# Optimization experiments

Hardware: AMD Instinct MI355X
Metric: run time of the kernel (lower is better)

Reference implementation:

```python
import jax, jax.numpy as jnp
import numpy as np

N_HEAD = 12
D_HEAD = 64


def setup_inputs() -> dict:
    key = jax.random.key(0)
    ks = jax.random.split(key, 9)
    bs, seq, d_model = 4, 2048, 768
    sc = 1.0 / np.sqrt(d_model)
    return {
        "q": jax.random.normal(ks[0], (bs, seq, d_model), jnp.float32),
        "k": jax.random.normal(ks[1], (bs, seq, d_model), jnp.float32),
        "v": jax.random.normal(ks[2], (bs, seq, d_model), jnp.float32),
        "Wq": jax.random.normal(ks[3], (d_model, d_model), jnp.float32) * sc,
        "bq": jax.random.normal(ks[4], (d_model,), jnp.float32) * 0.01,
        "Wk": jax.random.normal(ks[5], (d_model, d_model), jnp.float32) * sc,
        "bk": jax.random.normal(ks[6], (d_model,), jnp.float32) * 0.01,
        "Wv": jax.random.normal(ks[7], (d_model, d_model), jnp.float32) * sc,
        "bv": jax.random.normal(ks[8], (d_model,), jnp.float32) * 0.01,
    }


def _split_heads(x):
    # [bs, seq, n_head*d_head] -> [bs, n_head, seq, d_head]
    bs, seq, _ = x.shape
    return x.reshape(bs, seq, N_HEAD, D_HEAD).transpose(0, 2, 1, 3)


def reference(q, k, v, Wq, bq, Wk, bk, Wv, bv):
    # Linear projections (torch Linear: x @ W.T + b)
    wq = _split_heads(q @ Wq.T + bq)
    wk = _split_heads(k @ Wk.T + bk)
    wv = _split_heads(v @ Wv.T + bv)
    # scale=False in defaults -> raw dot products, no mask, dropout is eval no-op
    scores = jnp.einsum("bhqd,bhkd->bhqk", wq, wk)  # [bs, h, S, S]
    probs = jax.nn.softmax(scores, axis=-1)
    attn_vec = jnp.einsum("bhqk,bhkd->bhqd", probs, wv)
    bs, _, seq, _ = attn_vec.shape
    # merge heads -> [bs, seq, n_head*d_head]
    return attn_vec.transpose(0, 2, 1, 3).reshape(bs, seq, N_HEAD * D_HEAD)
```

## Files before the change

kernel.cpp:

```cpp
#include <hip/hip_runtime.h>
#include <stdint.h>

typedef _Float16 half8  __attribute__((ext_vector_type(8)));
typedef _Float16 half4v __attribute__((ext_vector_type(4)));
typedef float    floatx4 __attribute__((ext_vector_type(4)));

#define LOG2E 1.44269504088896340736f

__device__ __forceinline__ void gl_lds16(const _Float16* g, _Float16* l) {
  __builtin_amdgcn_global_load_lds(
      (__attribute__((address_space(1))) void*)g,
      (__attribute__((address_space(3))) void*)l, 16, 0, 0);
}

__device__ __forceinline__ half4v pack4(float a, float b, float c, float d) {
  auto lo = __builtin_amdgcn_cvt_pkrtz(a, b);
  auto hi = __builtin_amdgcn_cvt_pkrtz(c, d);
  return half4v{static_cast<_Float16>(lo[0]), static_cast<_Float16>(lo[1]),
                static_cast<_Float16>(hi[0]), static_cast<_Float16>(hi[1])};
}

struct CvtArgs {
  const float* sx[3];
  const float* sw[3];
  _Float16*    dx;
  _Float16*    dw;
};

__global__ void cvt_kernel(CvtArgs a) {
  const int z  = blockIdx.y;
  const int bx = blockIdx.x;
  const float* src;
  _Float16*    dst;
  int base;
  if (bx < 3072) { src = a.sx[z]; dst = a.dx + (size_t)z * 6291456; base = bx * 2048; }
  else           { src = a.sw[z]; dst = a.dw + (size_t)z * 589824;  base = (bx - 3072) * 2048; }
  const int i = base + threadIdx.x * 8;
  const float4* s = (const float4*)(src + i);
  float4 v0 = s[0], v1 = s[1];
  half8 h = { (_Float16)v0.x, (_Float16)v0.y, (_Float16)v0.z, (_Float16)v0.w,
              (_Float16)v1.x, (_Float16)v1.y, (_Float16)v1.z, (_Float16)v1.w };
  *(half8*)(dst + i) = h;
}


__device__ __forceinline__ void gemm_stage16(const _Float16* __restrict__ P,
                                             _Float16* sb, int r0, int k0, int tid) {
  #pragma unroll
  for (int i = 0; i < 2; ++i) {
    int G = i * 256 + tid;
    int r = G >> 2, gl = G & 3;
    int g = gl ^ ((r >> 1) & 3);
    gl_lds16(P + (size_t)(r0 + r) * 768 + k0 + g * 8, sb + G * 8);
  }
}

template <int RB, int WB, int VM, bool PREF>
__device__ __forceinline__ void gemm_body(
    int kpre, const _Float16* __restrict__ X, const _Float16* __restrict__ W,
    _Float16* As, _Float16* Bs, int m0, int n0, int tid, int z,
    int wr, int wc, int qd, int col, floatx4 (&acc)[4][4])
{
  asm volatile("s_waitcnt vmcnt(%0)" :: "i"(VM) : "memory");
  __builtin_amdgcn_s_barrier();
  __builtin_amdgcn_sched_barrier(0);
  if (PREF) {
    gemm_stage16(X, As + WB * 4096, m0, kpre, tid);
    gemm_stage16(W, Bs + WB * 4096, n0, kpre, tid);
  }
  __builtin_amdgcn_sched_barrier(0);

  half8 af[4], bf[4];
  #pragma unroll
  for (int t = 0; t < 4; ++t) {
    int ra = wr * 64 + t * 16 + col;
    af[t] = *(const half8*)(As + RB * 4096 + ra * 32 + ((qd ^ ((ra >> 1) & 3)) * 8));
  }
  #pragma unroll
  for (int t = 0; t < 4; ++t) {
    int rb = wc * 64 + t * 16 + col;
    bf[t] = *(const half8*)(Bs + RB * 4096 + rb * 32 + ((qd ^ ((rb >> 1) & 3)) * 8));
  }
  if (z == 2) {
    #pragma unroll
    for (int i = 0; i < 4; ++i)
      #pragma unroll
      for (int j = 0; j < 4; ++j)
        acc[i][j] = __builtin_amdgcn_mfma_f32_16x16x32_f16(af[i], bf[j], acc[i][j], 0, 0, 0);
  } else {
    #pragma unroll
    for (int i = 0; i < 4; ++i)
      #pragma unroll
      for (int j = 0; j < 4; ++j)
        acc[i][j] = __builtin_amdgcn_mfma_f32_16x16x32_f16(bf[j], af[i], acc[i][j], 0, 0, 0);
  }
}

__global__ __launch_bounds__(256, 2) void qkv_gemm(
    const _Float16* __restrict__ xh,
    const _Float16* __restrict__ wh,
    const float* __restrict__ bqp, const float* __restrict__ bkp, const float* __restrict__ bvp,
    _Float16* __restrict__ oq, _Float16* __restrict__ ok, _Float16* __restrict__ ovt)
{
  __shared__ __attribute__((aligned(16))) char smem[49152];
  _Float16* As = (_Float16*)smem;
  _Float16* Bs = (_Float16*)(smem + 24576);
  _Float16* Es = (_Float16*)smem;

  const int flat = blockIdx.x;
  const int z    = flat / 384;
  const int f    = flat % 384;
  const int xcd  = f & 7;
  const int slot = f >> 3;
  const int n0 = (slot % 6) * 128;
  const int m0 = (xcd + 8 * (slot / 6)) * 128;

  const _Float16* X = xh + (size_t)z * 6291456;
  const _Float16* W = wh + (size_t)z * 589824;
  const int tid  = threadIdx.x;
  const int lane = tid & 63, wid = tid >> 6;
  const int wr = wid >> 1, wc = wid & 1;
  const int qd = lane >> 4, col = lane & 15;

  const floatx4 z4 = {0.f, 0.f, 0.f, 0.f};
  floatx4 acc[4][4];
  #pragma unroll
  for (int i = 0; i < 4; ++i)
    #pragma unroll
    for (int j = 0; j < 4; ++j) acc[i][j] = z4;

  gemm_stage16(X, As,        m0, 0,  tid);
  gemm_stage16(W, Bs,        n0, 0,  tid);
  gemm_stage16(X, As + 4096, m0, 32, tid);
  gemm_stage16(W, Bs + 4096, n0, 32, tid);

  int jn = 64;
  #pragma unroll 1
  for (int it = 0; it < 7; ++it) {
    gemm_body<0, 2, 4, true>(jn,      X, W, As, Bs, m0, n0, tid, z, wr, wc, qd, col, acc);
    gemm_body<1, 0, 4, true>(jn + 32, X, W, As, Bs, m0, n0, tid, z, wr, wc, qd, col, acc);
    gemm_body<2, 1, 4, true>(jn + 64, X, W, As, Bs, m0, n0, tid, z, wr, wc, qd, col, acc);
    jn += 96;
  }
  gemm_body<0, 2, 4, true >(736, X, W, As, Bs, m0, n0, tid, z, wr, wc, qd, col, acc);
  gemm_body<1, 0, 4, false>(0,   X, W, As, Bs, m0, n0, tid, z, wr, wc, qd, col, acc);
  gemm_body<2, 1, 0, false>(0,   X, W, As, Bs, m0, n0, tid, z, wr, wc, qd, col, acc);

  __syncthreads();

  const float* bias = (z == 0) ? bqp : ((z == 1) ? bkp : bvp);
  const int b = m0 >> 11, s0 = m0 & 2047;
  if (z == 2) {
    #pragma unroll
    for (int j = 0; j < 4; ++j) {
      int n_loc = wc * 64 + j * 16 + col;
      float bb = bias[n0 + n_loc];
      #pragma unroll
      for (int i = 0; i < 4; ++i) {
        int s_loc = wr * 64 + i * 16 + qd * 4;
        half4v h = pack4(acc[i][j][0] + bb, acc[i][j][1] + bb,
                         acc[i][j][2] + bb, acc[i][j][3] + bb);
        *(half4v*)(Es + n_loc * 160 + s_loc) = h;
      }
    }
    __syncthreads();
    #pragma unroll
    for (int it = 0; it < 8; ++it) {
      int row = it * 16 + (tid >> 4);
      int k   = tid & 15;
      half8 vr = *(const half8*)(Es + row * 160 + k * 8);
      *(half8*)(ovt + ((size_t)(b * 768 + n0 + row)) * 2048 + s0 + k * 8) = vr;
    }
  } else {
    _Float16* O = (z == 0) ? oq : ok;
    const float scale = (z == 0) ? LOG2E : 1.0f;
    #pragma unroll
    for (int j = 0; j < 4; ++j) {
      int n_loc = wc * 64 + j * 16 + qd * 4;
      float4 bb = *(const float4*)(bias + n0 + n_loc);
      #pragma unroll
      for (int i = 0; i < 4; ++i) {
        int s_loc = wr * 64 + i * 16 + col;
        half4v h = pack4((acc[i][j][0] + bb.x) * scale, (acc[i][j][1] + bb.y) * scale,
                         (acc[i][j][2] + bb.z) * scale, (acc[i][j][3] + bb.w) * scale);
        *(half4v*)(Es + s_loc * 160 + n_loc) = h;
      }
    }
    __syncthreads();
    const int hh0 = n0 >> 6;
    #pragma unroll
    for (int it = 0; it < 8; ++it) {
      int seg = it * 32 + (tid >> 3);
      int s = seg >> 1, hseg = seg & 1;
      int k = tid & 7;
      half8 vr = *(const half8*)(Es + s * 160 + hseg * 64 + k * 8);
      int mb = (m0 + s) >> 11, sg = (m0 + s) & 2047;
      *(half8*)(O + (size_t)(mb * 12 + hh0 + hseg) * 131072
                  + (size_t)sg * 64 + k * 8) = vr;
    }
  }
}


__device__ __forceinline__ void issue_panel(const float* __restrict__ P,
                                            int r0, int k0, int tid,
                                            float4& a0, float4& a1,
                                            float4& b0, float4& b1) {
  {
    int G = tid;
    int r = G >> 2, gl = G & 3;
    int g = gl ^ ((r >> 1) & 3);
    const float4* s = (const float4*)(P + (size_t)(r0 + r) * 768 + k0 + g * 8);
    a0 = s[0]; a1 = s[1];
  }
  {
    int G = 256 + tid;
    int r = G >> 2, gl = G & 3;
    int g = gl ^ ((r >> 1) & 3);
    const float4* s = (const float4*)(P + (size_t)(r0 + r) * 768 + k0 + g * 8);
    b0 = s[0]; b1 = s[1];
  }
}

__device__ __forceinline__ void write_panel(_Float16* sb, int tid,
                                            const float4& a0, const float4& a1,
                                            const float4& b0, const float4& b1) {
  half8 h0 = { (_Float16)a0.x, (_Float16)a0.y, (_Float16)a0.z, (_Float16)a0.w,
               (_Float16)a1.x, (_Float16)a1.y, (_Float16)a1.z, (_Float16)a1.w };
  *(half8*)(sb + tid * 8) = h0;
  half8 h1 = { (_Float16)b0.x, (_Float16)b0.y, (_Float16)b0.z, (_Float16)b0.w,
               (_Float16)b1.x, (_Float16)b1.y, (_Float16)b1.z, (_Float16)b1.w };
  *(half8*)(sb + (256 + tid) * 8) = h1;
}

template <int BUF>
__device__ __forceinline__ void gemm_body_f32(
    int knext, const float* __restrict__ X, const float* __restrict__ W,
    _Float16* As, _Float16* Bs, int m0, int n0, int tid, int z,
    int wr, int wc, int qd, int col, floatx4 (&acc)[4][4])
{
  const bool pref = (knext < 768);
  float4 xa0, xa1, xb0, xb1, wa0, wa1, wb0, wb1;
  if (pref) {
    issue_panel(X, m0, knext, tid, xa0, xa1, xb0, xb1);
    issue_panel(W, n0, knext, tid, wa0, wa1, wb0, wb1);
  }

  half8 af[4], bf[4];
  #pragma unroll
  for (int t = 0; t < 4; ++t) {
    int ra = wr * 64 + t * 16 + col;
    af[t] = *(const half8*)(As + BUF * 4096 + ra * 32 + ((qd ^ ((ra >> 1) & 3)) * 8));
  }
  #pragma unroll
  for (int t = 0; t < 4; ++t) {
    int rb = wc * 64 + t * 16 + col;
    bf[t] = *(const half8*)(Bs + BUF * 4096 + rb * 32 + ((qd ^ ((rb >> 1) & 3)) * 8));
  }
  if (z == 2) {
    #pragma unroll
    for (int i = 0; i < 4; ++i)
      #pragma unroll
      for (int j = 0; j < 4; ++j)
        acc[i][j] = __builtin_amdgcn_mfma_f32_16x16x32_f16(af[i], bf[j], acc[i][j], 0, 0, 0);
  } else {
    #pragma unroll
    for (int i = 0; i < 4; ++i)
      #pragma unroll
      for (int j = 0; j < 4; ++j)
        acc[i][j] = __builtin_amdgcn_mfma_f32_16x16x32_f16(bf[j], af[i], acc[i][j], 0, 0, 0);
  }

  if (pref) {
    write_panel(As + (1 - BUF) * 4096, tid, xa0, xa1, xb0, xb1);
    write_panel(Bs + (1 - BUF) * 4096, tid, wa0, wa1, wb0, wb1);
  }
  __syncthreads();
}

__global__ __launch_bounds__(256, 2) void qkv_gemm_f32(
    const float* __restrict__ qx, const float* __restrict__ kx, const float* __restrict__ vx,
    const float* __restrict__ Wqp, const float* __restrict__ Wkp, const float* __restrict__ Wvp,
    const float* __restrict__ bqp, const float* __restrict__ bkp, const float* __restrict__ bvp,
    _Float16* __restrict__ oq, _Float16* __restrict__ ok, _Float16* __restrict__ ovt)
{
  __shared__ __attribute__((aligned(16))) char smem[40960];
  _Float16* As = (_Float16*)smem;
  _Float16* Bs = (_Float16*)(smem + 16384);
  _Float16* Es = (_Float16*)smem;

  const int tid  = threadIdx.x;
  const int lane = tid & 63, wid = tid >> 6;
  const int wr = wid >> 1, wc = wid & 1;
  const int qd = lane >> 4, col = lane & 15;

  #pragma unroll 1
  for (int t = blockIdx.x; t < 1152; t += 512) {
    const int m0 = (t & 63) * 128;
    const int n0 = ((t >> 6) % 6) * 128;
    const int z  = t / 384;
    const float* X = (z == 0) ? qx : ((z == 1) ? kx : vx);
    const float* W = (z == 0) ? Wqp : ((z == 1) ? Wkp : Wvp);

    const floatx4 z4 = {0.f, 0.f, 0.f, 0.f};
    floatx4 acc[4][4];
    #pragma unroll
    for (int i = 0; i < 4; ++i)
      #pragma unroll
      for (int j = 0; j < 4; ++j) acc[i][j] = z4;

    {
      float4 xa0, xa1, xb0, xb1, wa0, wa1, wb0, wb1;
      issue_panel(X, m0, 0, tid, xa0, xa1, xb0, xb1);
      issue_panel(W, n0, 0, tid, wa0, wa1, wb0, wb1);
      __syncthreads();
      write_panel(As, tid, xa0, xa1, xb0, xb1);
      write_panel(Bs, tid, wa0, wa1, wb0, wb1);
    }
    __syncthreads();
    for (int kk = 0; kk < 768; kk += 64) {
      gemm_body_f32<0>(kk + 32, X, W, As, Bs, m0, n0, tid, z, wr, wc, qd, col, acc);
      gemm_body_f32<1>(kk + 64, X, W, As, Bs, m0, n0, tid, z, wr, wc, qd, col, acc);
    }

    const float* bias = (z == 0) ? bqp : ((z == 1) ? bkp : bvp);
    const int b = m0 >> 11, s0 = m0 & 2047;
    if (z == 2) {
      #pragma unroll
      for (int j = 0; j < 4; ++j) {
        int n_loc = wc * 64 + j * 16 + col;
        float bb = bias[n0 + n_loc];
        #pragma unroll
        for (int i = 0; i < 4; ++i) {
          int s_loc = wr * 64 + i * 16 + qd * 4;
          half4v h = pack4(acc[i][j][0] + bb, acc[i][j][1] + bb,
                           acc[i][j][2] + bb, acc[i][j][3] + bb);
          *(half4v*)(Es + n_loc * 160 + s_loc) = h;
        }
      }
      __syncthreads();
      #pragma unroll
      for (int it = 0; it < 8; ++it) {
        int row = it * 16 + (tid >> 4);
        int k   = tid & 15;
        half8 vr = *(const half8*)(Es + row * 160 + k * 8);
        *(half8*)(ovt + ((size_t)(b * 768 + n0 + row)) * 2048 + s0 + k * 8) = vr;
      }
    } else {
      _Float16* O = (z == 0) ? oq : ok;
      const float scale = (z == 0) ? LOG2E : 1.0f;
      #pragma unroll
      for (int j = 0; j < 4; ++j) {
        int n_loc = wc * 64 + j * 16 + qd * 4;
        float4 bb = *(const float4*)(bias + n0 + n_loc);
        #pragma unroll
        for (int i = 0; i < 4; ++i) {
          int s_loc = wr * 64 + i * 16 + col;
          half4v h = pack4((acc[i][j][0] + bb.x) * scale, (acc[i][j][1] + bb.y) * scale,
                           (acc[i][j][2] + bb.z) * scale, (acc[i][j][3] + bb.w) * scale);
          *(half4v*)(Es + s_loc * 160 + n_loc) = h;
        }
      }
      __syncthreads();
      const int hh0 = n0 >> 6;
      #pragma unroll
      for (int it = 0; it < 8; ++it) {
        int seg = it * 32 + (tid >> 3);
        int s = seg >> 1, hseg = seg & 1;
        int k = tid & 7;
        half8 vr = *(const half8*)(Es + s * 160 + hseg * 64 + k * 8);
        int mb = (m0 + s) >> 11, sg = (m0 + s) & 2047;
        *(half8*)(O + (size_t)(mb * 12 + hh0 + hseg) * 131072
                    + (size_t)sg * 64 + k * 8) = vr;
      }
    }
  }
}


__device__ __forceinline__ void stage_kv(const _Float16* __restrict__ Kg,
                                         const _Float16* __restrict__ Vg,
                                         _Float16* ksd, _Float16* vsd, int j0, int tid) {
  #pragma unroll
  for (int i = 0; i < 2; ++i) {
    int c = i * 256 + tid;
    int row = c >> 3, sc = c & 7;
    gl_lds16(Kg + (size_t)(j0 + row) * 64 + ((sc ^ (row & 7)) * 8), ksd + c * 8);
    gl_lds16(Vg + (size_t)row * 2048 + j0 + ((sc ^ (row & 7)) * 8), vsd + c * 8);
  }
}

template <int BUF>
__device__ __forceinline__ void attn_body(
    int jnext, const _Float16* __restrict__ Kg, const _Float16* __restrict__ Vg,
    _Float16* Ks, _Float16* Vs, int tid,
    const half8 (&qf)[2][2], int kb0, int kb1, const int (&vb)[4],
    floatx4 (&negm)[2], floatx4 (&ol)[2], floatx4 (&o)[4][2])
{
  if (jnext < 2048)
    stage_kv(Kg, Vg, Ks + (1 - BUF) * 4096, Vs + (1 - BUF) * 4096, jnext, tid);

  const char* ksb = (const char*)Ks;
  const char* vsb = (const char*)Vs;

  floatx4 st[4][2];
  #pragma unroll
  for (int t = 0; t < 4; ++t) {
    half8 kf0 = *(const half8*)(ksb + BUF * 8192 + t * 2048 + kb0);
    half8 kf1 = *(const half8*)(ksb + BUF * 8192 + t * 2048 + kb1);
    #pragma unroll
    for (int qt = 0; qt < 2; ++qt) {
      st[t][qt] = __builtin_amdgcn_mfma_f32_16x16x32_f16(kf0, qf[qt][0], negm[qt], 0, 0, 0);
      st[t][qt] = __builtin_amdgcn_mfma_f32_16x16x32_f16(kf1, qf[qt][1], st[t][qt], 0, 0, 0);
    }
  }

  float mr[2];
  #pragma unroll
  for (int qt = 0; qt < 2; ++qt) {
    float v = fmaxf(
        fmaxf(fmaxf(fmaxf(st[0][qt][0], st[0][qt][1]), fmaxf(st[0][qt][2], st[0][qt][3])),
              fmaxf(fmaxf(st[1][qt][0], st[1][qt][1]), fmaxf(st[1][qt][2], st[1][qt][3]))),
        fmaxf(fmaxf(fmaxf(st[2][qt][0], st[2][qt][1]), fmaxf(st[2][qt][2], st[2][qt][3])),
              fmaxf(fmaxf(st[3][qt][0], st[3][qt][1]), fmaxf(st[3][qt][2], st[3][qt][3]))));
    v = fmaxf(v, __shfl_xor(v, 16, 64));
    v = fmaxf(v, __shfl_xor(v, 32, 64));
    mr[qt] = fmaxf(v, 0.f);
  }

  half4v pf[4][2];
  #pragma unroll
  for (int qt = 0; qt < 2; ++qt)
    #pragma unroll
    for (int t = 0; t < 4; ++t)
      pf[t][qt] = pack4(__builtin_amdgcn_exp2f(st[t][qt][0] - mr[qt]),
                        __builtin_amdgcn_exp2f(st[t][qt][1] - mr[qt]),
                        __builtin_amdgcn_exp2f(st[t][qt][2] - mr[qt]),
                        __builtin_amdgcn_exp2f(st[t][qt][3] - mr[qt]));

  if (__any(mr[0] > 0.f || mr[1] > 0.f)) {
    #pragma unroll
    for (int qt = 0; qt < 2; ++qt) {
      float al = __builtin_amdgcn_exp2f(-mr[qt]);
      negm[qt] -= mr[qt];
      ol[qt] *= al;
      #pragma unroll
      for (int dt = 0; dt < 4; ++dt) o[dt][qt] *= al;
    }
  }

  const half4v vone = {(_Float16)1.0f, (_Float16)1.0f, (_Float16)1.0f, (_Float16)1.0f};
  #pragma unroll
  for (int dt = 0; dt < 4; ++dt) {
    #pragma unroll
    for (int t = 0; t < 4; ++t) {
      half4v vf = *(const half4v*)(vsb + BUF * 8192 + dt * 2048 + vb[t]);
      #pragma unroll
      for (int qt = 0; qt < 2; ++qt)
        o[dt][qt] = __builtin_amdgcn_mfma_f32_16x16x16f16(vf, pf[t][qt], o[dt][qt], 0, 0, 0);
    }
  }
  #pragma unroll
  for (int t = 0; t < 4; ++t)
    #pragma unroll
    for (int qt = 0; qt < 2; ++qt)
      ol[qt] = __builtin_amdgcn_mfma_f32_16x16x16f16(vone, pf[t][qt], ol[qt], 0, 0, 0);

  __syncthreads();
}

__global__ __launch_bounds__(256, 3) void attn_kernel(
    const _Float16* __restrict__ Qm,
    const _Float16* __restrict__ Km,
    const _Float16* __restrict__ Vt,
    float* __restrict__ out)
{
  __shared__ __attribute__((aligned(16))) _Float16 Ks[2 * 4096];
  __shared__ __attribute__((aligned(16))) _Float16 Vs[2 * 4096];
  const int bh = blockIdx.x;
  const int q0 = blockIdx.y * 128;
  const int tid = threadIdx.x, lane = tid & 63, w = tid >> 6;
  const int qd = lane >> 4, col = lane & 15, c7 = col & 7;
  const _Float16* Qg = Qm + (size_t)bh * 131072;
  const _Float16* Kg = Km + (size_t)bh * 131072;
  const _Float16* Vg = Vt + (size_t)bh * 131072;

  half8 qf[2][2];
  #pragma unroll
  for (int qt = 0; qt < 2; ++qt)
    #pragma unroll
    for (int ks = 0; ks < 2; ++ks)
      qf[qt][ks] = *(const half8*)(Qg + (size_t)(q0 + w * 32 + qt * 16 + col) * 64
                                   + (ks * 4 + qd) * 8);

  const int kb0 = col * 128 + ((qd ^ c7) * 16);
  const int kb1 = col * 128 + (((4 + qd) ^ c7) * 16);
  const int vq = (qd >> 1) ^ c7;
  int vb[4];
  #pragma unroll
  for (int t = 0; t < 4; ++t)
    vb[t] = col * 128 + (qd & 1) * 8 + ((vq ^ (2 * t)) * 16);

  floatx4 negm[2] = {{100.f, 100.f, 100.f, 100.f}, {100.f, 100.f, 100.f, 100.f}};
  const floatx4 z4 = {0.f, 0.f, 0.f, 0.f};
  floatx4 ol[2] = {z4, z4};
  floatx4 o[4][2];
  #pragma unroll
  for (int dt = 0; dt < 4; ++dt)
    #pragma unroll
    for (int qt = 0; qt < 2; ++qt) o[dt][qt] = z4;

  stage_kv(Kg, Vg, Ks, Vs, 0, tid);
  __syncthreads();

  for (int jj = 0; jj < 2048; jj += 128) {
    attn_body<0>(jj + 64,  Kg, Vg, Ks, Vs, tid, qf, kb0, kb1, vb, negm, ol, o);
    attn_body<1>(jj + 128, Kg, Vg, Ks, Vs, tid, qf, kb0, kb1, vb, negm, ol, o);
  }

  const int b = bh / 12, h = bh % 12;
  #pragma unroll
  for (int qt = 0; qt < 2; ++qt) {
    float inv = 1.0f / ol[qt][0];
    int qg = q0 + w * 32 + qt * 16 + col;
    float* obase = out + ((size_t)b * 2048 + qg) * 768 + h * 64;
    #pragma unroll
    for (int dt = 0; dt < 4; ++dt) {
      floatx4 v = o[dt][qt];
      v *= inv;
      *(floatx4*)(obase + dt * 16 + qd * 4) = v;
    }
  }
}

extern "C" void kernel_launch(void* const* d_in, const int* in_sizes, int n_in,
                              void* d_out, int out_size, void* d_ws, size_t ws_size,
                              hipStream_t stream) {
  const float* q  = (const float*)d_in[0];
  const float* k  = (const float*)d_in[1];
  const float* v  = (const float*)d_in[2];
  const float* Wq = (const float*)d_in[3];
  const float* bq = (const float*)d_in[4];
  const float* Wk = (const float*)d_in[5];
  const float* bk = (const float*)d_in[6];
  const float* Wv = (const float*)d_in[7];
  const float* bv = (const float*)d_in[8];

  const size_t NX = 6291456;
  const size_t NW = 589824;
  const size_t need_full = (6 * NX + 3 * NW) * sizeof(_Float16);
  const size_t need_min  = (3 * NX) * sizeof(_Float16);

  if (ws_size >= need_full) {
    _Float16* xh = (_Float16*)d_ws;
    _Float16* wh = xh + 3 * NX;
    _Float16* qh = wh + 3 * NW;
    _Float16* kh = qh + NX;
    _Float16* vt = kh + NX;

    CvtArgs ca;
    ca.sx[0] = q;  ca.sx[1] = k;  ca.sx[2] = v;
    ca.sw[0] = Wq; ca.sw[1] = Wk; ca.sw[2] = Wv;
    ca.dx = xh; ca.dw = wh;

    cvt_kernel<<<dim3(3360, 3), 256, 0, stream>>>(ca);
    qkv_gemm<<<dim3(1152), 256, 0, stream>>>(xh, wh, bq, bk, bv, qh, kh, vt);
    attn_kernel<<<dim3(48, 16), 256, 0, stream>>>(qh, kh, vt, (float*)d_out);
  } else if (ws_size >= need_min) {
    _Float16* qh = (_Float16*)d_ws;
    _Float16* kh = qh + NX;
    _Float16* vt = kh + NX;
    qkv_gemm_f32<<<dim3(512), 256, 0, stream>>>(q, k, v, Wq, Wk, Wv, bq, bk, bv, qh, kh, vt);
    attn_kernel<<<dim3(48, 16), 256, 0, stream>>>(qh, kh, vt, (float*)d_out);
  }
}
```

Before: 248.5 us.

## Switch attention inner loop to 32x32x16 MFMA tiles with lane-shuffled P fragments

Rewrites the flash-attention inner loop so each wave computes its 32-query tile with 32x32x16 f16 MFMAs instead of 16x16 tiles. The exponentiated scores are packed into half8 operands by exchanging halves across lanes 32 apart, and the running max reduction needs one fewer shuffle. The aim is higher MFMA throughput per instruction and fewer LDS fragment loads and reduction steps. In exchange it adds cross-lane shuffles for P, uses larger accumulators that raise register pressure, and lowers the launch-bounds occupancy hint from 3 to 2.

```diff
diff --git a/kernel.cpp b/kernel.cpp
--- a/kernel.cpp
+++ b/kernel.cpp
@@ -3,7 +3,9 @@
 
 typedef _Float16 half8  __attribute__((ext_vector_type(8)));
 typedef _Float16 half4v __attribute__((ext_vector_type(4)));
+typedef __fp16   fp16x2 __attribute__((ext_vector_type(2)));
 typedef float    floatx4 __attribute__((ext_vector_type(4)));
+typedef float    floatx16 __attribute__((ext_vector_type(16)));
 
 #define LOG2E 1.44269504088896340736f
 
@@ -390,86 +392,91 @@
   }
 }
 
+__device__ __forceinline__ half8 make_pf(const float* e, int hi) {
+  union W { fp16x2 h; unsigned int u; };
+  W A, B, C, D;
+  A.h = __builtin_amdgcn_cvt_pkrtz(e[0], e[1]);
+  B.h = __builtin_amdgcn_cvt_pkrtz(e[2], e[3]);
+  C.h = __builtin_amdgcn_cvt_pkrtz(e[4], e[5]);
+  D.h = __builtin_amdgcn_cvt_pkrtz(e[6], e[7]);
+  unsigned int Ax = __shfl_xor(A.u, 32, 64);
+  unsigned int Bx = __shfl_xor(B.u, 32, 64);
+  unsigned int Cx = __shfl_xor(C.u, 32, 64);
+  unsigned int Dx = __shfl_xor(D.u, 32, 64);
+  union R { unsigned int w[4]; half8 v; } r;
+  r.w[0] = hi ? Cx : A.u;
+  r.w[1] = hi ? Dx : B.u;
+  r.w[2] = hi ? C.u : Ax;
+  r.w[3] = hi ? D.u : Bx;
+  return r.v;
+}
+
+__device__ __forceinline__ void attn_sub32(
+    const char* ksb, const char* vsb, int vb0, int vb1, int hi,
+    const half8 (&qf)[4], const int (&kvb)[4], const half8& vone,
+    float& nm, floatx16& lac, floatx16 (&o)[2])
+{
+  floatx16 st;
+  #pragma unroll
+  for (int i = 0; i < 16; ++i) st[i] = nm;
+  #pragma unroll
+  for (int ds = 0; ds < 4; ++ds) {
+    half8 kf = *(const half8*)(ksb + kvb[ds]);
+    st = __builtin_amdgcn_mfma_f32_32x32x16_f16(kf, qf[ds], st, 0, 0, 0);
+  }
+
+  float m0 = fmaxf(fmaxf(st[0], st[1]),  fmaxf(st[2], st[3]));
+  float m1 = fmaxf(fmaxf(st[4], st[5]),  fmaxf(st[6], st[7]));
+  float m2 = fmaxf(fmaxf(st[8], st[9]),  fmaxf(st[10], st[11]));
+  float m3 = fmaxf(fmaxf(st[12], st[13]), fmaxf(st[14], st[15]));
+  float v = fmaxf(fmaxf(m0, m1), fmaxf(m2, m3));
+  v = fmaxf(v, __shfl_xor(v, 32, 64));
+  float mr = fmaxf(v, 0.f);
+
+  float e[16];
+  #pragma unroll
+  for (int i = 0; i < 16; ++i) e[i] = __builtin_amdgcn_exp2f(st[i] - mr);
+
+  if (__any(mr > 0.f)) {
+    float al = __builtin_amdgcn_exp2f(-mr);
+    nm -= mr;
+    lac *= al;
+    o[0] *= al;
+    o[1] *= al;
+  }
+
+  half8 pfA = make_pf(e, hi);
+  half8 pfB = make_pf(e + 8, hi);
+
+  #pragma unroll
+  for (int dt = 0; dt < 2; ++dt) {
+    half8 vf0 = *(const half8*)(vsb + dt * 4096 + vb0);
+    o[dt] = __builtin_amdgcn_mfma_f32_32x32x16_f16(vf0, pfA, o[dt], 0, 0, 0);
+    half8 vf1 = *(const half8*)(vsb + dt * 4096 + vb1);
+    o[dt] = __builtin_amdgcn_mfma_f32_32x32x16_f16(vf1, pfB, o[dt], 0, 0, 0);
+  }
+  lac = __builtin_amdgcn_mfma_f32_32x32x16_f16(vone, pfA, lac, 0, 0, 0);
+  lac = __builtin_amdgcn_mfma_f32_32x32x16_f16(vone, pfB, lac, 0, 0, 0);
+}
+
 template <int BUF>
 __device__ __forceinline__ void attn_body(
     int jnext, const _Float16* __restrict__ Kg, const _Float16* __restrict__ Vg,
-    _Float16* Ks, _Float16* Vs, int tid,
-    const half8 (&qf)[2][2], int kb0, int kb1, const int (&vb)[4],
-    floatx4 (&negm)[2], floatx4 (&ol)[2], floatx4 (&o)[4][2])
+    _Float16* Ks, _Float16* Vs, int tid, int hi,
+    const half8 (&qf)[4], const int (&kvb)[4], const half8& vone,
+    float& nm, floatx16& lac, floatx16 (&o)[2])
 {
   if (jnext < 2048)
     stage_kv(Kg, Vg, Ks + (1 - BUF) * 4096, Vs + (1 - BUF) * 4096, jnext, tid);
 
-  const char* ksb = (const char*)Ks;
-  const char* vsb = (const char*)Vs;
-
-  floatx4 st[4][2];
-  #pragma unroll
-  for (int t = 0; t < 4; ++t) {
-    half8 kf0 = *(const half8*)(ksb + BUF * 8192 + t * 2048 + kb0);
-    half8 kf1 = *(const half8*)(ksb + BUF * 8192 + t * 2048 + kb1);
-    #pragma unroll
-    for (int qt = 0; qt < 2; ++qt) {
-      st[t][qt] = __builtin_amdgcn_mfma_f32_16x16x32_f16(kf0, qf[qt][0], negm[qt], 0, 0, 0);
-      st[t][qt] = __builtin_amdgcn_mfma_f32_16x16x32_f16(kf1, qf[qt][1], st[t][qt], 0, 0, 0);
-    }
-  }
-
-  float mr[2];
-  #pragma unroll
-  for (int qt = 0; qt < 2; ++qt) {
-    float v = fmaxf(
-        fmaxf(fmaxf(fmaxf(st[0][qt][0], st[0][qt][1]), fmaxf(st[0][qt][2], st[0][qt][3])),
-              fmaxf(fmaxf(st[1][qt][0], st[1][qt][1]), fmaxf(st[1][qt][2], st[1][qt][3]))),
-        fmaxf(fmaxf(fmaxf(st[2][qt][0], st[2][qt][1]), fmaxf(st[2][qt][2], st[2][qt][3])),
-              fmaxf(fmaxf(st[3][qt][0], st[3][qt][1]), fmaxf(st[3][qt][2], st[3][qt][3]))));
-    v = fmaxf(v, __shfl_xor(v, 16, 64));
-    v = fmaxf(v, __shfl_xor(v, 32, 64));
-    mr[qt] = fmaxf(v, 0.f);
-  }
-
-  half4v pf[4][2];
-  #pragma unroll
-  for (int qt = 0; qt < 2; ++qt)
-    #pragma unroll
-    for (int t = 0; t < 4; ++t)
-      pf[t][qt] = pack4(__builtin_amdgcn_exp2f(st[t][qt][0] - mr[qt]),
-                        __builtin_amdgcn_exp2f(st[t][qt][1] - mr[qt]),
-                        __builtin_amdgcn_exp2f(st[t][qt][2] - mr[qt]),
-                        __builtin_amdgcn_exp2f(st[t][qt][3] - mr[qt]));
-
-  if (__any(mr[0] > 0.f || mr[1] > 0.f)) {
-    #pragma unroll
-    for (int qt = 0; qt < 2; ++qt) {
-      float al = __builtin_amdgcn_exp2f(-mr[qt]);
-      negm[qt] -= mr[qt];
-      ol[qt] *= al;
-      #pragma unroll
-      for (int dt = 0; dt < 4; ++dt) o[dt][qt] *= al;
-    }
-  }
-
-  const half4v vone = {(_Float16)1.0f, (_Float16)1.0f, (_Float16)1.0f, (_Float16)1.0f};
-  #pragma unroll
-  for (int dt = 0; dt < 4; ++dt) {
-    #pragma unroll
-    for (int t = 0; t < 4; ++t) {
-      half4v vf = *(const half4v*)(vsb + BUF * 8192 + dt * 2048 + vb[t]);
-      #pragma unroll
-      for (int qt = 0; qt < 2; ++qt)
-        o[dt][qt] = __builtin_amdgcn_mfma_f32_16x16x16f16(vf, pf[t][qt], o[dt][qt], 0, 0, 0);
-    }
-  }
-  #pragma unroll
-  for (int t = 0; t < 4; ++t)
-    #pragma unroll
-    for (int qt = 0; qt < 2; ++qt)
-      ol[qt] = __builtin_amdgcn_mfma_f32_16x16x16f16(vone, pf[t][qt], ol[qt], 0, 0, 0);
-
+  const char* ksb = (const char*)Ks + BUF * 8192;
+  const char* vsb = (const char*)Vs + BUF * 8192;
+  attn_sub32(ksb,        vsb, kvb[0], kvb[1], hi, qf, kvb, vone, nm, lac, o);
+  attn_sub32(ksb + 4096, vsb, kvb[2], kvb[3], hi, qf, kvb, vone, nm, lac, o);
   __syncthreads();
 }
 
-__global__ __launch_bounds__(256, 3) void attn_kernel(
+__global__ __launch_bounds__(256, 2) void attn_kernel(
     const _Float16* __restrict__ Qm,
     const _Float16* __restrict__ Km,
     const _Float16* __restrict__ Vt,
@@ -480,57 +487,50 @@
   const int bh = blockIdx.x;
   const int q0 = blockIdx.y * 128;
   const int tid = threadIdx.x, lane = tid & 63, w = tid >> 6;
-  const int qd = lane >> 4, col = lane & 15, c7 = col & 7;
+  const int lq = lane & 31, hi = lane >> 5, c7 = lq & 7;
+  const int qrow = q0 + w * 32 + lq;
   const _Float16* Qg = Qm + (size_t)bh * 131072;
   const _Float16* Kg = Km + (size_t)bh * 131072;
   const _Float16* Vg = Vt + (size_t)bh * 131072;
 
-  half8 qf[2][2];
-  #pragma unroll
-  for (int qt = 0; qt < 2; ++qt)
-    #pragma unroll
-    for (int ks = 0; ks < 2; ++ks)
-      qf[qt][ks] = *(const half8*)(Qg + (size_t)(q0 + w * 32 + qt * 16 + col) * 64
-                                   + (ks * 4 + qd) * 8);
-
-  const int kb0 = col * 128 + ((qd ^ c7) * 16);
-  const int kb1 = col * 128 + (((4 + qd) ^ c7) * 16);
-  const int vq = (qd >> 1) ^ c7;
-  int vb[4];
-  #pragma unroll
-  for (int t = 0; t < 4; ++t)
-    vb[t] = col * 128 + (qd & 1) * 8 + ((vq ^ (2 * t)) * 16);
-
-  floatx4 negm[2] = {{100.f, 100.f, 100.f, 100.f}, {100.f, 100.f, 100.f, 100.f}};
-  const floatx4 z4 = {0.f, 0.f, 0.f, 0.f};
-  floatx4 ol[2] = {z4, z4};
-  floatx4 o[4][2];
-  #pragma unroll
-  for (int dt = 0; dt < 4; ++dt)
-    #pragma unroll
-    for (int qt = 0; qt < 2; ++qt) o[dt][qt] = z4;
+  half8 qf[4];
+  #pragma unroll
+  for (int ds = 0; ds < 4; ++ds)
+    qf[ds] = *(const half8*)(Qg + (size_t)qrow * 64 + ds * 16 + hi * 8);
+
+  int kvb[4];
+  #pragma unroll
+  for (int j = 0; j < 4; ++j)
+    kvb[j] = lq * 128 + (((j * 2 + hi) ^ c7) * 16);
+
+  const half8 vone = {(_Float16)1.0f, (_Float16)1.0f, (_Float16)1.0f, (_Float16)1.0f,
+                      (_Float16)1.0f, (_Float16)1.0f, (_Float16)1.0f, (_Float16)1.0f};
+
+  float nm = 100.f;
+  floatx16 lac;
+  floatx16 o[2];
+  #pragma unroll
+  for (int i = 0; i < 16; ++i) { lac[i] = 0.f; o[0][i] = 0.f; o[1][i] = 0.f; }
 
   stage_kv(Kg, Vg, Ks, Vs, 0, tid);
   __syncthreads();
 
   for (int jj = 0; jj < 2048; jj += 128) {
-    attn_body<0>(jj + 64,  Kg, Vg, Ks, Vs, tid, qf, kb0, kb1, vb, negm, ol, o);
-    attn_body<1>(jj + 128, Kg, Vg, Ks, Vs, tid, qf, kb0, kb1, vb, negm, ol, o);
+    attn_body<0>(jj + 64,  Kg, Vg, Ks, Vs, tid, hi, qf, kvb, vone, nm, lac, o);
+    attn_body<1>(jj + 128, Kg, Vg, Ks, Vs, tid, hi, qf, kvb, vone, nm, lac, o);
   }
 
   const int b = bh / 12, h = bh % 12;
-  #pragma unroll
-  for (int qt = 0; qt < 2; ++qt) {
-    float inv = 1.0f / ol[qt][0];
-    int qg = q0 + w * 32 + qt * 16 + col;
-    float* obase = out + ((size_t)b * 2048 + qg) * 768 + h * 64;
-    #pragma unroll
-    for (int dt = 0; dt < 4; ++dt) {
-      floatx4 v = o[dt][qt];
-      v *= inv;
-      *(floatx4*)(obase + dt * 16 + qd * 4) = v;
-    }
-  }
+  const float inv = 1.0f / lac[0];
+  float* obase = out + ((size_t)b * 2048 + qrow) * 768 + h * 64;
+  #pragma unroll
+  for (int dt = 0; dt < 2; ++dt)
+    #pragma unroll
+    for (int rq = 0; rq < 4; ++rq) {
+      floatx4 vv = { o[dt][4 * rq + 0] * inv, o[dt][4 * rq + 1] * inv,
+                     o[dt][4 * rq + 2] * inv, o[dt][4 * rq + 3] * inv };
+      *(floatx4*)(obase + dt * 32 + rq * 8 + hi * 4) = vv;
+    }
 }
 
 extern "C" void kernel_launch(void* const* d_in, const int* in_sizes, int n_in,
```

Measured after the change: 257.1 us. 1.03x slower.
